# Performance work log

Measured on AMD Instinct MI355X. Metric: run time of the kernel, lower is better.

Reference implementation:

```python
import jax, jax.numpy as jnp
import numpy as np

N = 30000      # particles
E = 300000     # directed edges
H = 128        # hidden size
L = 10         # GNN layers
EMB = 16       # particle-type embedding size
T = 5          # velocity history window
NTYPES = 9
RADIUS = 0.05
OUT = 2
NODE_IN = 2 * T + 4 + EMB  # 30


def _mlp_ln(x, W1, b1, W2, b2, W3, b3, g, be):
    # Linear-ReLU-Linear-ReLU-Linear-LayerNorm (matches node/edge encoders and GraphNet blocks)
    h = jax.nn.relu(x @ W1 + b1)
    h = jax.nn.relu(h @ W2 + b2)
    h = h @ W3 + b3
    mu = jnp.mean(h, axis=-1, keepdims=True)
    var = jnp.mean((h - mu) ** 2, axis=-1, keepdims=True)
    return (h - mu) * jax.lax.rsqrt(var + 1e-5) * g + be


def setup_inputs() -> dict:
    key = jax.random.key(0)
    ks = iter(jax.random.split(key, 48))
    nx = lambda: next(ks)
    inp = {}
    inp["vel"] = jax.random.normal(nx(), (N, T, 2), jnp.float32) * 0.01
    inp["pos"] = jax.random.uniform(nx(), (N, 2), dtype=jnp.float32)
    inp["bounds"] = jnp.array([[0.0, 1.0], [0.0, 1.0]], jnp.float32)  # [dim, (lo,hi)]
    inp["tgt_pos"] = jax.random.uniform(nx(), (N, 2), dtype=jnp.float32)
    inp["particle_type"] = jax.random.randint(nx(), (N,), 0, NTYPES, jnp.int32)
    inp["nonk_mask"] = jax.random.randint(nx(), (N,), 0, 2, jnp.int32)
    inp["senders"] = jax.random.randint(nx(), (E,), 0, N, jnp.int32)
    inp["receivers"] = jax.random.randint(nx(), (E,), 0, N, jnp.int32)
    inp["emb"] = jax.random.normal(nx(), (NTYPES, EMB), jnp.float32) * 0.1

    def mlp_p(pre, din, lead=()):
        w = lambda i, o: jax.random.normal(nx(), lead + (i, o), jnp.float32) / np.sqrt(i)
        inp[pre + "_W1"] = w(din, H); inp[pre + "_b1"] = jnp.zeros(lead + (H,), jnp.float32)
        inp[pre + "_W2"] = w(H, H);   inp[pre + "_b2"] = jnp.zeros(lead + (H,), jnp.float32)
        inp[pre + "_W3"] = w(H, H);   inp[pre + "_b3"] = jnp.zeros(lead + (H,), jnp.float32)
        inp[pre + "_g"] = jnp.ones(lead + (H,), jnp.float32)
        inp[pre + "_be"] = jnp.zeros(lead + (H,), jnp.float32)

    mlp_p("ne", NODE_IN)          # node encoder
    mlp_p("ee", 3)                # edge encoder
    mlp_p("ge", 3 * H, (L,))      # per-layer edge-update MLPs
    mlp_p("gn", 2 * H, (L,))      # per-layer node-update MLPs
    inp["de_W1"] = jax.random.normal(nx(), (H, H), jnp.float32) / np.sqrt(H)
    inp["de_b1"] = jnp.zeros((H,), jnp.float32)
    inp["de_W2"] = jax.random.normal(nx(), (H, H), jnp.float32) / np.sqrt(H)
    inp["de_b2"] = jnp.zeros((H,), jnp.float32)
    inp["de_W3"] = jax.random.normal(nx(), (H, OUT), jnp.float32) / np.sqrt(H)
    inp["de_b3"] = jnp.zeros((OUT,), jnp.float32)
    return inp


def reference(vel, pos, bounds, tgt_pos, particle_type, nonk_mask, senders, receivers, emb,
              ne_W1, ne_b1, ne_W2, ne_b2, ne_W3, ne_b3, ne_g, ne_be,
              ee_W1, ee_b1, ee_W2, ee_b2, ee_W3, ee_b3, ee_g, ee_be,
              ge_W1, ge_b1, ge_W2, ge_b2, ge_W3, ge_b3, ge_g, ge_be,
              gn_W1, gn_b1, gn_W2, gn_b2, gn_W3, gn_b3, gn_g, gn_be,
              de_W1, de_b1, de_W2, de_b2, de_W3, de_b3):
    n = pos.shape[0]
    # --- construct node features ---
    vels = vel.reshape(n, -1)                                   # [N, T*2]
    dtw = jnp.concatenate([pos - bounds[:, 0], bounds[:, 1] - pos], axis=1)
    dtw = jnp.clip(dtw / RADIUS, -1.0, 1.0)                     # [N, 4]
    type_emb = emb[particle_type]                               # [N, EMB] gather
    node_attr = jnp.concatenate([vels, dtw, type_emb], axis=1)  # [N, 30]
    # --- construct edge features (senders/receivers precomputed; KD-tree is CPU-side) ---
    dist_vec = (pos[senders] - pos[receivers]) / RADIUS         # [E, 2]
    dist = jnp.linalg.norm(dist_vec, axis=1, keepdims=True)     # [E, 1]
    edge_attr = jnp.concatenate([dist_vec, dist], axis=1)       # [E, 3]
    # --- encode ---
    nodes = _mlp_ln(node_attr, ne_W1, ne_b1, ne_W2, ne_b2, ne_W3, ne_b3, ne_g, ne_be)
    edges = _mlp_ln(edge_attr, ee_W1, ee_b1, ee_W2, ee_b2, ee_W3, ee_b3, ee_g, ee_be)
    # --- process: L message-passing layers with residuals ---
    for l in range(ge_W1.shape[0]):
        e_in = jnp.concatenate([edges, nodes[senders], nodes[receivers]], axis=1)  # [E, 3H]
        edges = edges + _mlp_ln(e_in, ge_W1[l], ge_b1[l], ge_W2[l], ge_b2[l], ge_W3[l], ge_b3[l], ge_g[l], ge_be[l])
        agg = jax.ops.segment_sum(edges, receivers, num_segments=n)               # [N, H] scatter-add
        n_in = jnp.concatenate([nodes, agg], axis=1)                              # [N, 2H]
        nodes = nodes + _mlp_ln(n_in, gn_W1[l], gn_b1[l], gn_W2[l], gn_b2[l], gn_W3[l], gn_b3[l], gn_g[l], gn_be[l])
    # --- decode ---
    h = jax.nn.relu(nodes @ de_W1 + de_b1)
    h = jax.nn.relu(h @ de_W2 + de_b2)
    pred_acc = h @ de_W3 + de_b3                                 # [N, 2]
    # --- Euler integration step (out_size == 2 branch) ---
    pred_pos = pos + vel[:, -1, :] + pred_acc
    pred_pos = jnp.where(nonk_mask[:, None].astype(bool), pred_pos, tgt_pos)
    return pred_acc[:, None, :], pred_pos[:, None, :]
```

## Files before the change

kernel.cpp:

```cpp
#include <hip/hip_runtime.h>
#include <hip/hip_bf16.h>

typedef __hip_bfloat16 bf16;
typedef unsigned short u16;
typedef unsigned int u32;
typedef __attribute__((ext_vector_type(8))) short short8;
typedef __attribute__((ext_vector_type(4))) float f32x4;

#define NPART 30000
#define NEDGE 300000
#define HD 128
#define NLAYER 10
#define NFLOAT_ARRAYS 43
#define NMAT 66

__device__ __forceinline__ bool detect_bf16(const unsigned short* braw) {
    return braw[1] == 0x3F80u;
}

__device__ __forceinline__ u16 f2b(float f) {
    u32 u = __float_as_uint(f);
    u += 0x7FFFu + ((u >> 16) & 1u);
    return (u16)(u >> 16);
}
__device__ __forceinline__ u32 pack2(float a, float b) {
    return (u32)f2b(a) | ((u32)f2b(b) << 16);
}
__device__ __forceinline__ float b2flo(u32 u) { return __uint_as_float(u << 16); }
__device__ __forceinline__ float b2fhi(u32 u) { return __uint_as_float(u & 0xFFFF0000u); }

struct ConvArgs {
    const void* src[NFLOAT_ARRAYS];
    int n[NFLOAT_ARRAYS];
    int off[NFLOAT_ARRAYS];
};

__global__ __launch_bounds__(256)
void k_convert(ConvArgs a, float* __restrict__ dst, const unsigned short* __restrict__ braw)
{
    const bool isb = detect_bf16(braw);
    const int aid = blockIdx.y;
    const int n = a.n[aid];
    float* o = dst + a.off[aid];
    const int stride = gridDim.x * 256;
    int i = blockIdx.x * 256 + threadIdx.x;
    if (isb) {
        const unsigned short* s = (const unsigned short*)a.src[aid];
        for (; i < n; i += stride) {
            const unsigned int u = ((unsigned int)s[i]) << 16;
            o[i] = __uint_as_float(u);
        }
    } else {
        const float* s = (const float*)a.src[aid];
        for (; i < n; i += stride) o[i] = s[i];
    }
}

__global__ __launch_bounds__(256)
void k_hist(const int* __restrict__ rcv, int* __restrict__ counts)
{
    const int e = blockIdx.x * 256 + threadIdx.x;
    if (e < NEDGE) atomicAdd(&counts[rcv[e]], 1);
}

__global__ __launch_bounds__(1024)
void k_scan(const int* __restrict__ counts, int* __restrict__ row_ptr, int* __restrict__ cursor)
{
    __shared__ int part[1024];
    const int t = threadIdx.x;
    const int base = t * 32;
    int local[32];
    int s = 0;
#pragma unroll
    for (int k = 0; k < 32; k++) {
        const int idx = base + k;
        const int v = (idx < NPART) ? counts[idx] : 0;
        local[k] = s;
        s += v;
    }
    part[t] = s;
    __syncthreads();
    for (int off = 1; off < 1024; off <<= 1) {
        const int v = (t >= off) ? part[t - off] : 0;
        __syncthreads();
        part[t] += v;
        __syncthreads();
    }
    const int excl = (t == 0) ? 0 : part[t - 1];
#pragma unroll
    for (int k = 0; k < 32; k++) {
        const int idx = base + k;
        if (idx < NPART) {
            const int rp = excl + local[k];
            row_ptr[idx] = rp;
            cursor[idx] = rp;
        }
    }
    if (t == 0) row_ptr[NPART] = NEDGE;
}

__global__ __launch_bounds__(256)
void k_scatter(const int* __restrict__ snd, const int* __restrict__ rcv,
               int* __restrict__ cursor, int* __restrict__ snd_s, int* __restrict__ rcv_s)
{
    const int e = blockIdx.x * 256 + threadIdx.x;
    if (e < NEDGE) {
        const int r = rcv[e];
        const int p = atomicAdd(&cursor[r], 1);
        snd_s[p] = snd[e];
        rcv_s[p] = r;
    }
}

struct PackArgs {
    int src_off[NMAT];
    int dst_off[NMAT];
    int K[NMAT];
    int nks[NMAT];
};

__global__ __launch_bounds__(256)
void k_pack(const float* __restrict__ cw, u16* __restrict__ wpk, PackArgs pa)
{
    const int mid = blockIdx.y;
    const int nks = pa.nks[mid];
    const int total = nks * 4096;
    const int d = blockIdx.x * 256 + threadIdx.x;
    if (d >= total) return;
    const int j = d & 7, l = (d >> 3) & 63, t = d >> 9;
    const int ks = t % nks, mt = t / nks;
    const int hid = mt * 16 + (l & 15);
    const int k = ks * 32 + (l >> 4) * 8 + j;
    const float v = (k < pa.K[mid]) ? cw[pa.src_off[mid] + k * HD + hid] : 0.0f;
    wpk[pa.dst_off[mid] + d] = f2b(v);
}

template<int NKS, int XROW>
__device__ __forceinline__ void gemm16(const u16* __restrict__ Wp,
                                       const float* __restrict__ Bias,
                                       const u16* __restrict__ x,
                                       f32x4 acc[4][2],
                                       const int wm, const int wn,
                                       const int l15, const int lg, const int lane)
{
#pragma unroll
    for (int mt = 0; mt < 4; mt++) {
        const f32x4 bv = *(const f32x4*)(Bias + wm * 64 + mt * 16 + lg * 4);
        acc[mt][0] = bv;
        acc[mt][1] = bv;
    }
    const u16* xr0 = x + (wn * 32 + l15) * XROW + lg * 8;
    const u16* xr1 = xr0 + 16 * XROW;
    const u16* wp = Wp + (wm * 4 * NKS) * 512 + lane * 8;
#pragma unroll
    for (int ks = 0; ks < NKS; ks++) {
        const short8 b0 = *(const short8*)(xr0 + ks * 32);
        const short8 b1 = *(const short8*)(xr1 + ks * 32);
#pragma unroll
        for (int mt = 0; mt < 4; mt++) {
            const short8 a = *(const short8*)(wp + (mt * NKS + ks) * 512);
            acc[mt][0] = __builtin_amdgcn_mfma_f32_16x16x32_bf16(a, b0, acc[mt][0], 0, 0, 0);
            acc[mt][1] = __builtin_amdgcn_mfma_f32_16x16x32_bf16(a, b1, acc[mt][1], 0, 0, 0);
        }
    }
}

__device__ __forceinline__ void store_h(u16* __restrict__ h, const f32x4 acc[4][2],
                                        const int wm, const int wn, const int l15, const int lg)
{
#pragma unroll
    for (int nt = 0; nt < 2; nt++) {
        const int e = wn * 32 + nt * 16 + l15;
#pragma unroll
        for (int mt = 0; mt < 4; mt++) {
            const int hid = wm * 64 + mt * 16 + lg * 4;
            const f32x4 v = acc[mt][nt];
            const u32 lo = pack2(fmaxf(v[0], 0.0f), fmaxf(v[1], 0.0f));
            const u32 hi = pack2(fmaxf(v[2], 0.0f), fmaxf(v[3], 0.0f));
            *(uint2*)(h + e * 136 + hid) = make_uint2(lo, hi);
        }
    }
}

template<int NKS1, int XROW>
__device__ __forceinline__ void mlp_mfma(const u16* __restrict__ xs,
    u16* __restrict__ h1, u16* __restrict__ h2,
    float (*red)[2][2][16][2],
    const u16* __restrict__ W1p, const float* __restrict__ B1,
    const u16* __restrict__ W2p, const float* __restrict__ B2,
    const u16* __restrict__ W3p, const float* __restrict__ B3,
    const float* __restrict__ g, const float* __restrict__ be,
    float outv[4][2][4],
    const int wm, const int wn, const int l15, const int lg, const int lane)
{
    f32x4 acc[4][2];
    gemm16<NKS1, XROW>(W1p, B1, xs, acc, wm, wn, l15, lg, lane);
    __syncthreads();
    store_h(h1, acc, wm, wn, l15, lg);
    __syncthreads();
    gemm16<4, 136>(W2p, B2, h1, acc, wm, wn, l15, lg, lane);
    store_h(h2, acc, wm, wn, l15, lg);
    __syncthreads();
    gemm16<4, 136>(W3p, B3, h2, acc, wm, wn, l15, lg, lane);
    float ps[2], pss[2];
#pragma unroll
    for (int nt = 0; nt < 2; nt++) {
        float s = 0.0f, ss = 0.0f;
#pragma unroll
        for (int mt = 0; mt < 4; mt++) {
#pragma unroll
            for (int r = 0; r < 4; r++) {
                const float v = acc[mt][nt][r];
                s += v; ss += v * v;
            }
        }
        s += __shfl_xor(s, 16); ss += __shfl_xor(ss, 16);
        s += __shfl_xor(s, 32); ss += __shfl_xor(ss, 32);
        ps[nt] = s; pss[nt] = ss;
    }
    if (lane < 16) {
#pragma unroll
        for (int nt = 0; nt < 2; nt++) {
            red[wm][wn][nt][l15][0] = ps[nt];
            red[wm][wn][nt][l15][1] = pss[nt];
        }
    }
    __syncthreads();
#pragma unroll
    for (int nt = 0; nt < 2; nt++) {
        const float S  = red[0][wn][nt][l15][0] + red[1][wn][nt][l15][0];
        const float SS = red[0][wn][nt][l15][1] + red[1][wn][nt][l15][1];
        const float mu  = S * (1.0f / 128.0f);
        const float var = SS * (1.0f / 128.0f) - mu * mu;
        const float inv = rsqrtf(var + 1e-5f);
#pragma unroll
        for (int mt = 0; mt < 4; mt++) {
            const int hid = wm * 64 + mt * 16 + lg * 4;
            const f32x4 gv  = *(const f32x4*)(g + hid);
            const f32x4 bev = *(const f32x4*)(be + hid);
#pragma unroll
            for (int r = 0; r < 4; r++)
                outv[mt][nt][r] = (acc[mt][nt][r] - mu) * inv * gv[r] + bev[r];
        }
    }
}

__device__ __forceinline__ float nfeat(int i, int k,
    const float* __restrict__ vel, const float* __restrict__ pos,
    const float* __restrict__ bounds, const int* __restrict__ ptype,
    const float* __restrict__ emb)
{
    if (k < 10) return vel[i * 10 + k];
    if (k < 14) {
        const int q = k - 10;
        float sub;
        if (q < 2) sub = pos[i * 2 + q] - bounds[q * 2 + 0];
        else       sub = bounds[(q - 2) * 2 + 1] - pos[i * 2 + (q - 2)];
        const float dv = sub * 20.0f;
        return fminf(fmaxf(dv, -1.0f), 1.0f);
    }
    if (k < 30) return emb[ptype[i] * 16 + (k - 14)];
    return 0.0f;
}

__global__ __launch_bounds__(256)
void k_node_enc_m(const float* __restrict__ vel, const float* __restrict__ pos,
                  const float* __restrict__ bounds, const int* __restrict__ ptype,
                  const float* __restrict__ emb,
                  const u16* __restrict__ W1p, const float* __restrict__ B1,
                  const u16* __restrict__ W2p, const float* __restrict__ B2,
                  const u16* __restrict__ W3p, const float* __restrict__ B3,
                  const float* __restrict__ g, const float* __restrict__ be,
                  float* __restrict__ nodes, u16* __restrict__ nodes_bf)
{
    __shared__ __align__(16) u16 lds[17408];
    __shared__ float red[2][2][2][16][2];
    const int tid = threadIdx.x;
    const int i0 = blockIdx.x * 64;
    for (int idx = tid; idx < 1024; idx += 256) {
        const int m = idx >> 4, kk = idx & 15;
        const int i = i0 + m;
        float f0 = 0.0f, f1 = 0.0f;
        if (i < NPART) {
            f0 = nfeat(i, kk * 2 + 0, vel, pos, bounds, ptype, emb);
            f1 = nfeat(i, kk * 2 + 1, vel, pos, bounds, ptype, emb);
        }
        *(u32*)(lds + m * 40 + kk * 2) = pack2(f0, f1);
    }
    __syncthreads();
    const int lane = tid & 63, wv = tid >> 6;
    const int wm = wv >> 1, wn = wv & 1, l15 = lane & 15, lg = lane >> 4;
    float outv[4][2][4];
    mlp_mfma<1, 40>(lds, lds, lds + 8704, red, W1p, B1, W2p, B2, W3p, B3, g, be,
                    outv, wm, wn, l15, lg, lane);
#pragma unroll
    for (int nt = 0; nt < 2; nt++) {
        const int i = i0 + wn * 32 + nt * 16 + l15;
        if (i < NPART) {
#pragma unroll
            for (int mt = 0; mt < 4; mt++) {
                const int hid = wm * 64 + mt * 16 + lg * 4;
                const float4 v = make_float4(outv[mt][nt][0], outv[mt][nt][1],
                                             outv[mt][nt][2], outv[mt][nt][3]);
                *(float4*)(nodes + (size_t)i * HD + hid) = v;
                *(uint2*)(nodes_bf + (size_t)i * HD + hid) =
                    make_uint2(pack2(v.x, v.y), pack2(v.z, v.w));
            }
        }
    }
}

__global__ __launch_bounds__(256)
void k_edge_enc_m(const float* __restrict__ pos, const int* __restrict__ snd_s,
                  const int* __restrict__ rcv_s,
                  const u16* __restrict__ W1p, const float* __restrict__ B1,
                  const u16* __restrict__ W2p, const float* __restrict__ B2,
                  const u16* __restrict__ W3p, const float* __restrict__ B3,
                  const float* __restrict__ g, const float* __restrict__ be,
                  u16* __restrict__ edges_bf)
{
    __shared__ __align__(16) u16 lds[17408];
    __shared__ float red[2][2][2][16][2];
    const int tid = threadIdx.x;
    const int e0 = blockIdx.x * 64;
    for (int idx = tid; idx < 1024; idx += 256) {
        const int m = idx >> 4, kk = idx & 15;
        const int e = min(e0 + m, NEDGE - 1);
        u32 w = 0;
        if (kk < 2) {
            const int s = snd_s[e], r = rcv_s[e];
            const float dx = (pos[s * 2 + 0] - pos[r * 2 + 0]) * 20.0f;
            const float dy = (pos[s * 2 + 1] - pos[r * 2 + 1]) * 20.0f;
            if (kk == 0) w = pack2(dx, dy);
            else         w = pack2(sqrtf(dx * dx + dy * dy), 0.0f);
        }
        *(u32*)(lds + m * 40 + kk * 2) = w;
    }
    __syncthreads();
    const int lane = tid & 63, wv = tid >> 6;
    const int wm = wv >> 1, wn = wv & 1, l15 = lane & 15, lg = lane >> 4;
    float outv[4][2][4];
    mlp_mfma<1, 40>(lds, lds, lds + 8704, red, W1p, B1, W2p, B2, W3p, B3, g, be,
                    outv, wm, wn, l15, lg, lane);
#pragma unroll
    for (int nt = 0; nt < 2; nt++) {
        const int e = e0 + wn * 32 + nt * 16 + l15;
        if (e < NEDGE) {
#pragma unroll
            for (int mt = 0; mt < 4; mt++) {
                const int hid = wm * 64 + mt * 16 + lg * 4;
                *(uint2*)(edges_bf + (size_t)e * HD + hid) =
                    make_uint2(pack2(outv[mt][nt][0], outv[mt][nt][1]),
                               pack2(outv[mt][nt][2], outv[mt][nt][3]));
            }
        }
    }
}

__device__ __forceinline__ void egemm_seg32(const u16* __restrict__ Wp,
                                            const u16* __restrict__ x,
                                            f32x4 acc[2][2], const int ks0,
                                            const int wm,
                                            const int l15, const int lg, const int lane)
{
    const u16* xr0 = x + l15 * 136 + lg * 8;
    const u16* xr1 = xr0 + 16 * 136;
#pragma unroll
    for (int ks = 0; ks < 4; ks++) {
        const short8 b0 = *(const short8*)(xr0 + ks * 32);
        const short8 b1 = *(const short8*)(xr1 + ks * 32);
#pragma unroll
        for (int mt = 0; mt < 2; mt++) {
            const short8 a = *(const short8*)(Wp + (((wm * 2 + mt) * 12 + ks0 + ks) * 64 + lane) * 8);
            acc[mt][0] = __builtin_amdgcn_mfma_f32_16x16x32_bf16(a, b0, acc[mt][0], 0, 0, 0);
            acc[mt][1] = __builtin_amdgcn_mfma_f32_16x16x32_bf16(a, b1, acc[mt][1], 0, 0, 0);
        }
    }
}

__device__ __forceinline__ void egemm_h32(const u16* __restrict__ Wp,
                                          const float* __restrict__ Bias,
                                          const u16* __restrict__ x,
                                          f32x4 acc[2][2],
                                          const int wm,
                                          const int l15, const int lg, const int lane)
{
#pragma unroll
    for (int mt = 0; mt < 2; mt++) {
        const f32x4 bv = *(const f32x4*)(Bias + wm * 32 + mt * 16 + lg * 4);
        acc[mt][0] = bv;
        acc[mt][1] = bv;
    }
    const u16* xr0 = x + l15 * 136 + lg * 8;
    const u16* xr1 = xr0 + 16 * 136;
#pragma unroll
    for (int ks = 0; ks < 4; ks++) {
        const short8 b0 = *(const short8*)(xr0 + ks * 32);
        const short8 b1 = *(const short8*)(xr1 + ks * 32);
#pragma unroll
        for (int mt = 0; mt < 2; mt++) {
            const short8 a = *(const short8*)(Wp + (((wm * 2 + mt) * 4 + ks) * 64 + lane) * 8);
            acc[mt][0] = __builtin_amdgcn_mfma_f32_16x16x32_bf16(a, b0, acc[mt][0], 0, 0, 0);
            acc[mt][1] = __builtin_amdgcn_mfma_f32_16x16x32_bf16(a, b1, acc[mt][1], 0, 0, 0);
        }
    }
}

__device__ __forceinline__ void estore_h32(u16* __restrict__ h, const f32x4 acc[2][2],
                                           const int wm, const int l15, const int lg)
{
#pragma unroll
    for (int nt = 0; nt < 2; nt++) {
        const int row = nt * 16 + l15;
#pragma unroll
        for (int mt = 0; mt < 2; mt++) {
            const int hid = wm * 32 + mt * 16 + lg * 4;
            const f32x4 v = acc[mt][nt];
            const u32 lo = pack2(fmaxf(v[0], 0.0f), fmaxf(v[1], 0.0f));
            const u32 hi = pack2(fmaxf(v[2], 0.0f), fmaxf(v[3], 0.0f));
            *(uint2*)(h + row * 136 + hid) = make_uint2(lo, hi);
        }
    }
}

__global__ __launch_bounds__(256, 8)
void k_edge_layer_m(const u16* __restrict__ nodes_bf, u16* __restrict__ edges_bf,
                    float* __restrict__ agg,
                    const int* __restrict__ snd_s, const int* __restrict__ rcv_s,
                    const u16* __restrict__ W1p, const float* __restrict__ B1,
                    const u16* __restrict__ W2p, const float* __restrict__ B2,
                    const u16* __restrict__ W3p, const float* __restrict__ B3,
                    const float* __restrict__ g, const float* __restrict__ be)
{
    __shared__ __align__(16) u16 sb[2 * 4352];
    __shared__ float red[4][2][16][2];
    __shared__ int rblk[34];
    u16* b0 = sb;
    u16* b1 = sb + 4352;
    float* fout = (float*)sb;

    const int tid = threadIdx.x;
    const int e0 = blockIdx.x * 32;
    const int lane = tid & 63, wm = tid >> 6;
    const int l15 = lane & 15, lg = lane >> 4;

    if (tid < 32)       rblk[tid] = rcv_s[e0 + tid];
    else if (tid == 32) rblk[32] = (e0 > 0) ? rcv_s[e0 - 1] : -2;
    else if (tid == 33) rblk[33] = (e0 + 32 < NEDGE) ? rcv_s[e0 + 32] : -2;

    uint4 e_old[2];
#pragma unroll
    for (int t = 0; t < 2; t++) {
        const int idx = tid + t * 256;
        const int m = idx >> 4, q = idx & 15;
        e_old[t] = *(const uint4*)(edges_bf + (size_t)(e0 + m) * HD + q * 8);
        *(uint4*)(b0 + m * 136 + q * 8) = e_old[t];
    }
    uint4 st[2];
#pragma unroll
    for (int t = 0; t < 2; t++) {
        const int idx = tid + t * 256;
        const int m = idx >> 4, q = idx & 15;
        st[t] = *(const uint4*)(nodes_bf + (size_t)snd_s[e0 + m] * HD + q * 8);
    }
    __syncthreads();

    f32x4 acc[2][2];
#pragma unroll
    for (int mt = 0; mt < 2; mt++) {
        const f32x4 bv = *(const f32x4*)(B1 + wm * 32 + mt * 16 + lg * 4);
        acc[mt][0] = bv;
        acc[mt][1] = bv;
    }
    __builtin_amdgcn_s_setprio(1);
    egemm_seg32(W1p, b0, acc, 0, wm, l15, lg, lane);
    __builtin_amdgcn_s_setprio(0);
#pragma unroll
    for (int t = 0; t < 2; t++) {
        const int idx = tid + t * 256;
        const int m = idx >> 4, q = idx & 15;
        *(uint4*)(b1 + m * 136 + q * 8) = st[t];
    }
#pragma unroll
    for (int t = 0; t < 2; t++) {
        const int idx = tid + t * 256;
        const int m = idx >> 4, q = idx & 15;
        st[t] = *(const uint4*)(nodes_bf + (size_t)rcv_s[e0 + m] * HD + q * 8);
    }
    __syncthreads();

    __builtin_amdgcn_s_setprio(1);
    egemm_seg32(W1p, b1, acc, 4, wm, l15, lg, lane);
    __builtin_amdgcn_s_setprio(0);
#pragma unroll
    for (int t = 0; t < 2; t++) {
        const int idx = tid + t * 256;
        const int m = idx >> 4, q = idx & 15;
        *(uint4*)(b0 + m * 136 + q * 8) = st[t];
    }
    __syncthreads();

    __builtin_amdgcn_s_setprio(1);
    egemm_seg32(W1p, b0, acc, 8, wm, l15, lg, lane);
    __builtin_amdgcn_s_setprio(0);
    estore_h32(b1, acc, wm, l15, lg);
    __syncthreads();

    __builtin_amdgcn_s_setprio(1);
    egemm_h32(W2p, B2, b1, acc, wm, l15, lg, lane);
    __builtin_amdgcn_s_setprio(0);
    estore_h32(b0, acc, wm, l15, lg);
    __syncthreads();

    __builtin_amdgcn_s_setprio(1);
    egemm_h32(W3p, B3, b0, acc, wm, l15, lg, lane);
    __builtin_amdgcn_s_setprio(0);

    float ps[2], pss[2];
#pragma unroll
    for (int nt = 0; nt < 2; nt++) {
        float s = 0.0f, ss = 0.0f;
#pragma unroll
        for (int mt = 0; mt < 2; mt++) {
#pragma unroll
            for (int r = 0; r < 4; r++) {
                const float v = acc[mt][nt][r];
                s += v; ss += v * v;
            }
        }
        s += __shfl_xor(s, 16); ss += __shfl_xor(ss, 16);
        s += __shfl_xor(s, 32); ss += __shfl_xor(ss, 32);
        ps[nt] = s; pss[nt] = ss;
    }
    if (lane < 16) {
#pragma unroll
        for (int nt = 0; nt < 2; nt++) {
            red[wm][nt][l15][0] = ps[nt];
            red[wm][nt][l15][1] = pss[nt];
        }
    }
    __syncthreads();

#pragma unroll
    for (int nt = 0; nt < 2; nt++) {
        const float S  = red[0][nt][l15][0] + red[1][nt][l15][0]
                       + red[2][nt][l15][0] + red[3][nt][l15][0];
        const float SS = red[0][nt][l15][1] + red[1][nt][l15][1]
                       + red[2][nt][l15][1] + red[3][nt][l15][1];
        const float mu  = S * (1.0f / 128.0f);
        const float var = SS * (1.0f / 128.0f) - mu * mu;
        const float inv = rsqrtf(var + 1e-5f);
        const int row = nt * 16 + l15;
#pragma unroll
        for (int mt = 0; mt < 2; mt++) {
            const int hid = wm * 32 + mt * 16 + lg * 4;
            const f32x4 gv  = *(const f32x4*)(g + hid);
            const f32x4 bev = *(const f32x4*)(be + hid);
            f32x4 o;
#pragma unroll
            for (int r = 0; r < 4; r++)
                o[r] = (acc[mt][nt][r] - mu) * inv * gv[r] + bev[r];
            *(f32x4*)(fout + row * 132 + hid) = o;
        }
    }
    __syncthreads();

#pragma unroll
    for (int t = 0; t < 2; t++) {
        const int idx = tid + t * 256;
        const int m = idx >> 4, q = idx & 15;
        float4 lo = *(const float4*)(fout + m * 132 + q * 8);
        float4 hi = *(const float4*)(fout + m * 132 + q * 8 + 4);
        const uint4 o = e_old[t];
        lo.x += b2flo(o.x); lo.y += b2fhi(o.x);
        lo.z += b2flo(o.y); lo.w += b2fhi(o.y);
        hi.x += b2flo(o.z); hi.y += b2fhi(o.z);
        hi.z += b2flo(o.w); hi.w += b2fhi(o.w);
        *(float4*)(fout + m * 132 + q * 8) = lo;
        *(float4*)(fout + m * 132 + q * 8 + 4) = hi;
        *(uint4*)(edges_bf + (size_t)(e0 + m) * HD + q * 8) =
            make_uint4(pack2(lo.x, lo.y), pack2(lo.z, lo.w),
                       pack2(hi.x, hi.y), pack2(hi.z, hi.w));
    }
    __syncthreads();

    const int c = tid & 31;
    for (int ms = (tid >> 5); ms < 32; ms += 8) {
        const int rs = rblk[ms];
        if (ms > 0 && rblk[ms - 1] == rs) continue;
        int me = ms + 1;
        while (me < 32 && rblk[me] == rs) me++;
        float4 s = make_float4(0.0f, 0.0f, 0.0f, 0.0f);
        for (int m = ms; m < me; m++) {
            const float4 v = *(const float4*)(fout + m * 132 + c * 4);
            s.x += v.x; s.y += v.y; s.z += v.z; s.w += v.w;
        }
        float* ap = agg + (size_t)rs * HD + c * 4;
        const bool bnd = (ms == 0 && rblk[32] == rs) || (me == 32 && rblk[33] == rs);
        if (bnd) {
            atomicAdd(ap + 0, s.x); atomicAdd(ap + 1, s.y);
            atomicAdd(ap + 2, s.z); atomicAdd(ap + 3, s.w);
        } else {
            *(float4*)ap = s;
        }
    }
}

__global__ __launch_bounds__(256)
void k_node_layer_m(float* __restrict__ nodes, u16* __restrict__ nodes_bf,
                    float* __restrict__ agg,
                    const u16* __restrict__ W1p, const float* __restrict__ B1,
                    const u16* __restrict__ W2p, const float* __restrict__ B2,
                    const u16* __restrict__ W3p, const float* __restrict__ B3,
                    const float* __restrict__ g, const float* __restrict__ be)
{
    __shared__ __align__(16) u16 lds[17408];
    __shared__ float red[2][2][2][16][2];
    const int tid = threadIdx.x;
    const int i0 = blockIdx.x * 64;
    for (int idx = tid; idx < 1024; idx += 256) {
        const int m = idx >> 4, q = idx & 15;
        const int i = min(i0 + m, NPART - 1);
        const float* src = nodes + (size_t)i * HD + q * 8;
        const float4 a = *(const float4*)(src);
        const float4 b = *(const float4*)(src + 4);
        *(uint4*)(lds + m * 264 + q * 8) =
            make_uint4(pack2(a.x, a.y), pack2(a.z, a.w), pack2(b.x, b.y), pack2(b.z, b.w));
    }
    const float4 z4 = make_float4(0.0f, 0.0f, 0.0f, 0.0f);
    for (int idx = tid; idx < 1024; idx += 256) {
        const int m = idx >> 4, q = idx & 15;
        const int i = min(i0 + m, NPART - 1);
        float* src = agg + (size_t)i * HD + q * 8;
        const float4 a = *(const float4*)(src);
        const float4 b = *(const float4*)(src + 4);
        *(uint4*)(lds + m * 264 + 128 + q * 8) =
            make_uint4(pack2(a.x, a.y), pack2(a.z, a.w), pack2(b.x, b.y), pack2(b.z, b.w));
        *(float4*)(src) = z4;
        *(float4*)(src + 4) = z4;
    }
    __syncthreads();
    const int lane = tid & 63, wv = tid >> 6;
    const int wm = wv >> 1, wn = wv & 1, l15 = lane & 15, lg = lane >> 4;
    float outv[4][2][4];
    mlp_mfma<8, 264>(lds, lds, lds + 8704, red, W1p, B1, W2p, B2, W3p, B3, g, be,
                     outv, wm, wn, l15, lg, lane);
#pragma unroll
    for (int nt = 0; nt < 2; nt++) {
        const int i = i0 + wn * 32 + nt * 16 + l15;
        if (i < NPART) {
            float* np = nodes + (size_t)i * HD;
#pragma unroll
            for (int mt = 0; mt < 4; mt++) {
                const int hid = wm * 64 + mt * 16 + lg * 4;
                const float4 old = *(const float4*)(np + hid);
                const float4 nv = make_float4(old.x + outv[mt][nt][0],
                                              old.y + outv[mt][nt][1],
                                              old.z + outv[mt][nt][2],
                                              old.w + outv[mt][nt][3]);
                *(float4*)(np + hid) = nv;
                *(uint2*)(nodes_bf + (size_t)i * HD + hid) =
                    make_uint2(pack2(nv.x, nv.y), pack2(nv.z, nv.w));
            }
        }
    }
}

template<int K, int S>
__device__ __forceinline__ void gemv(const float* __restrict__ in,
                                     const float* __restrict__ W,
                                     const float* __restrict__ B,
                                     float acc[8])
{
    const int j = threadIdx.x;
    const float bb = B[j];
#pragma unroll
    for (int m = 0; m < 8; m++) acc[m] = bb;
    constexpr int K4 = (K / 4) * 4;
    for (int k = 0; k < K4; k += 4) {
        const float w0 = W[(k + 0) * HD + j];
        const float w1 = W[(k + 1) * HD + j];
        const float w2 = W[(k + 2) * HD + j];
        const float w3 = W[(k + 3) * HD + j];
#pragma unroll
        for (int m = 0; m < 8; m++) {
            const float4 x = *(const float4*)(in + m * S + k);
            float a = acc[m];
            a = fmaf(x.x, w0, a);
            a = fmaf(x.y, w1, a);
            a = fmaf(x.z, w2, a);
            a = fmaf(x.w, w3, a);
            acc[m] = a;
        }
    }
#pragma unroll
    for (int k = K4; k < K; k++) {
        const float w = W[k * HD + j];
#pragma unroll
        for (int m = 0; m < 8; m++) acc[m] = fmaf(in[m * S + k], w, acc[m]);
    }
}

__global__ __launch_bounds__(128)
void k_decoder(const float* __restrict__ nodes,
               const float* W1, const float* B1, const float* W2, const float* B2,
               const float* W3, const float* B3,
               const float* __restrict__ vel, const float* __restrict__ pos,
               const float* __restrict__ tgt, const int* __restrict__ nonk,
               const unsigned short* __restrict__ braw, void* __restrict__ d_out)
{
    __shared__ __align__(16) float xs[8 * HD];
    __shared__ __align__(16) float h1[8 * HD];
    __shared__ __align__(16) float h2[8 * HD];
    const int j = threadIdx.x;
    const int i0 = blockIdx.x * 8;
    float acc[8];
#pragma unroll
    for (int m = 0; m < 8; m++) xs[m * HD + j] = nodes[(i0 + m) * HD + j];
    __syncthreads();
    gemv<HD, HD>(xs, W1, B1, acc);
#pragma unroll
    for (int m = 0; m < 8; m++) h1[m * HD + j] = fmaxf(acc[m], 0.0f);
    __syncthreads();
    gemv<HD, HD>(h1, W2, B2, acc);
#pragma unroll
    for (int m = 0; m < 8; m++) h2[m * HD + j] = fmaxf(acc[m], 0.0f);
    __syncthreads();
    if (j < 16) {
        const int m = j >> 1, d = j & 1, i = i0 + m;
        float a = B3[d];
        for (int k = 0; k < HD; k++) a = fmaf(h2[m * HD + k], W3[k * 2 + d], a);
        float pp = pos[i * 2 + d] + vel[i * 10 + 8 + d] + a;
        if (nonk[i] == 0) pp = tgt[i * 2 + d];
        if (detect_bf16(braw)) {
            bf16* o = (bf16*)d_out;
            o[i * 2 + d] = __float2bfloat16(a);
            o[2 * NPART + i * 2 + d] = __float2bfloat16(pp);
        } else {
            float* o = (float*)d_out;
            o[i * 2 + d] = a;
            o[2 * NPART + i * 2 + d] = pp;
        }
    }
}

extern "C" void kernel_launch(void* const* d_in, const int* in_sizes, int n_in,
                              void* d_out, int out_size, void* d_ws, size_t ws_size,
                              hipStream_t stream)
{
    const int* ptype = (const int*)d_in[4];
    const int* nonk  = (const int*)d_in[5];
    const int* snd   = (const int*)d_in[6];
    const int* rcv   = (const int*)d_in[7];
    const unsigned short* braw = (const unsigned short*)d_in[2];

    int fmap[NFLOAT_ARRAYS];
    {
        int c = 0;
        fmap[c++] = 0; fmap[c++] = 1; fmap[c++] = 2; fmap[c++] = 3; fmap[c++] = 8;
        for (int i = 9; i <= 46; i++) fmap[c++] = i;
    }
    ConvArgs ca;
    const float* fp[47];
    float* cw = (float*)d_ws;
    int off = 0;
    for (int i = 0; i < NFLOAT_ARRAYS; i++) {
        ca.src[i] = d_in[fmap[i]];
        ca.n[i]   = in_sizes[fmap[i]];
        ca.off[i] = off;
        fp[fmap[i]] = cw + off;
        off += in_sizes[fmap[i]];
    }
    float* nodes = cw + ((off + 3) & ~3);
    float* agg   = nodes + (size_t)NPART * HD;
    u16* edges_bf = (u16*)(agg + (size_t)NPART * HD);
    u16* nodes_bf = edges_bf + (size_t)NEDGE * HD;
    u16* wpk = nodes_bf + (size_t)NPART * HD;

    PackArgs pa;
    int dst = 0, c = 0;
    int pk[NMAT];
    auto addm = [&](long srcoff, int K) {
        const int nk = (K + 31) / 32;
        pa.src_off[c] = (int)srcoff;
        pa.K[c] = K;
        pa.nks[c] = nk;
        pa.dst_off[c] = dst;
        pk[c] = dst;
        dst += nk * 4096;
        c++;
    };
    addm(fp[9]  - cw, 30);  addm(fp[11] - cw, 128); addm(fp[13] - cw, 128);
    addm(fp[17] - cw, 3);   addm(fp[19] - cw, 128); addm(fp[21] - cw, 128);
    for (int l = 0; l < NLAYER; l++) {
        addm(fp[25] - cw + (long)l * 384 * HD, 384);
        addm(fp[27] - cw + (long)l * HD * HD, 128);
        addm(fp[29] - cw + (long)l * HD * HD, 128);
    }
    for (int l = 0; l < NLAYER; l++) {
        addm(fp[33] - cw + (long)l * 256 * HD, 256);
        addm(fp[35] - cw + (long)l * HD * HD, 128);
        addm(fp[37] - cw + (long)l * HD * HD, 128);
    }

    int* ip = (int*)(wpk + ((dst + 7) & ~7));
    int* row_ptr = ip;            ip += NPART + 8;
    int* cursor  = ip;            ip += NPART;
    int* counts  = ip;            ip += NPART;
    int* snd_s   = ip;            ip += NEDGE;
    int* rcv_s   = ip;

    const int EBL = (NEDGE + 255) / 256;

    k_convert<<<dim3(64, NFLOAT_ARRAYS), 256, 0, stream>>>(ca, cw, braw);
    hipMemsetAsync(counts, 0, (size_t)NPART * sizeof(int), stream);
    hipMemsetAsync(agg, 0, (size_t)NPART * HD * sizeof(float), stream);
    k_hist<<<EBL, 256, 0, stream>>>(rcv, counts);
    k_scan<<<1, 1024, 0, stream>>>(counts, row_ptr, cursor);
    k_scatter<<<EBL, 256, 0, stream>>>(snd, rcv, cursor, snd_s, rcv_s);
    k_pack<<<dim3(192, NMAT), 256, 0, stream>>>(cw, wpk, pa);

    const int NB = (NPART + 63) / 64;
    const int EB = (NEDGE + 63) / 64;
    const int EB32 = NEDGE / 32;

    k_node_enc_m<<<NB, 256, 0, stream>>>(fp[0], fp[1], fp[2], ptype, fp[8],
        wpk + pk[0], fp[10], wpk + pk[1], fp[12], wpk + pk[2], fp[14],
        fp[15], fp[16], nodes, nodes_bf);
    k_edge_enc_m<<<EB, 256, 0, stream>>>(fp[1], snd_s, rcv_s,
        wpk + pk[3], fp[18], wpk + pk[4], fp[20], wpk + pk[5], fp[22],
        fp[23], fp[24], edges_bf);

    for (int l = 0; l < NLAYER; l++) {
        k_edge_layer_m<<<EB32, 256, 0, stream>>>(nodes_bf, edges_bf, agg, snd_s, rcv_s,
            wpk + pk[6 + 3 * l],  fp[26] + (size_t)l * HD,
            wpk + pk[7 + 3 * l],  fp[28] + (size_t)l * HD,
            wpk + pk[8 + 3 * l],  fp[30] + (size_t)l * HD,
            fp[31] + (size_t)l * HD, fp[32] + (size_t)l * HD);
        k_node_layer_m<<<NB, 256, 0, stream>>>(nodes, nodes_bf, agg,
            wpk + pk[36 + 3 * l], fp[34] + (size_t)l * HD,
            wpk + pk[37 + 3 * l], fp[36] + (size_t)l * HD,
            wpk + pk[38 + 3 * l], fp[38] + (size_t)l * HD,
            fp[39] + (size_t)l * HD, fp[40] + (size_t)l * HD);
    }

    k_decoder<<<NPART / 8, 128, 0, stream>>>(nodes,
        fp[41], fp[42], fp[43], fp[44], fp[45], fp[46],
        fp[0], fp[1], fp[3], nonk, braw, d_out);
}
```

Baseline: 2.219 ms.

## Replace boundary atomics with per-block partial buffers reduced in node kernel

The edge-layer kernel writes receiver segments that cross its 32-edge block boundary into a per-block boundary buffer instead of using atomicAdd into agg. The node kernel uses row_ptr to decide whether a node's sum lives in agg or must be assembled from the boundary partials of consecutive blocks. Because every agg slot is now either overwritten or ignored, the per-layer zeroing of agg and the initial memset go away. This removes float atomics and the zeroing stores, at the cost of an extra row_ptr lookup and branchy reduction in the node kernel.

```diff
diff --git a/kernel.cpp b/kernel.cpp
--- a/kernel.cpp
+++ b/kernel.cpp
@@ -425,7 +425,7 @@
 
 __global__ __launch_bounds__(256, 8)
 void k_edge_layer_m(const u16* __restrict__ nodes_bf, u16* __restrict__ edges_bf,
-                    float* __restrict__ agg,
+                    float* __restrict__ agg, float* __restrict__ bnd,
                     const int* __restrict__ snd_s, const int* __restrict__ rcv_s,
                     const u16* __restrict__ W1p, const float* __restrict__ B1,
                     const u16* __restrict__ W2p, const float* __restrict__ B2,
@@ -595,20 +595,19 @@
             const float4 v = *(const float4*)(fout + m * 132 + c * 4);
             s.x += v.x; s.y += v.y; s.z += v.z; s.w += v.w;
         }
-        float* ap = agg + (size_t)rs * HD + c * 4;
-        const bool bnd = (ms == 0 && rblk[32] == rs) || (me == 32 && rblk[33] == rs);
-        if (bnd) {
-            atomicAdd(ap + 0, s.x); atomicAdd(ap + 1, s.y);
-            atomicAdd(ap + 2, s.z); atomicAdd(ap + 3, s.w);
-        } else {
-            *(float4*)ap = s;
-        }
+        const bool extb = (ms == 0 && rblk[32] == rs);
+        const bool extf = (me == 32 && rblk[33] == rs);
+        float* ap;
+        if (!extb && !extf) ap = agg + (size_t)rs * HD + c * 4;
+        else ap = bnd + ((size_t)blockIdx.x * 2 + (extb ? 0 : 1)) * HD + c * 4;
+        *(float4*)ap = s;
     }
 }
 
 __global__ __launch_bounds__(256)
 void k_node_layer_m(float* __restrict__ nodes, u16* __restrict__ nodes_bf,
-                    float* __restrict__ agg,
+                    const float* __restrict__ agg, const float* __restrict__ bnd,
+                    const int* __restrict__ row_ptr,
                     const u16* __restrict__ W1p, const float* __restrict__ B1,
                     const u16* __restrict__ W2p, const float* __restrict__ B2,
                     const u16* __restrict__ W3p, const float* __restrict__ B3,
@@ -616,8 +615,11 @@
 {
     __shared__ __align__(16) u16 lds[17408];
     __shared__ float red[2][2][2][16][2];
+    __shared__ int rp[65];
     const int tid = threadIdx.x;
     const int i0 = blockIdx.x * 64;
+    if (tid < 65) rp[tid] = row_ptr[min(i0 + tid, NPART)];
+    __syncthreads();
     for (int idx = tid; idx < 1024; idx += 256) {
         const int m = idx >> 4, q = idx & 15;
         const int i = min(i0 + m, NPART - 1);
@@ -627,17 +629,35 @@
         *(uint4*)(lds + m * 264 + q * 8) =
             make_uint4(pack2(a.x, a.y), pack2(a.z, a.w), pack2(b.x, b.y), pack2(b.z, b.w));
     }
-    const float4 z4 = make_float4(0.0f, 0.0f, 0.0f, 0.0f);
     for (int idx = tid; idx < 1024; idx += 256) {
         const int m = idx >> 4, q = idx & 15;
-        const int i = min(i0 + m, NPART - 1);
-        float* src = agg + (size_t)i * HD + q * 8;
-        const float4 a = *(const float4*)(src);
-        const float4 b = *(const float4*)(src + 4);
+        const int i = i0 + m;
+        float4 a = make_float4(0.0f, 0.0f, 0.0f, 0.0f);
+        float4 b = make_float4(0.0f, 0.0f, 0.0f, 0.0f);
+        if (i < NPART) {
+            const int p0 = rp[m], p1 = rp[m + 1];
+            if (p1 > p0) {
+                const int b0 = p0 >> 5, b1 = (p1 - 1) >> 5;
+                if (b0 == b1) {
+                    const float* src = agg + (size_t)i * HD + q * 8;
+                    a = *(const float4*)(src);
+                    b = *(const float4*)(src + 4);
+                } else {
+                    const float* s1 = bnd + ((size_t)b0 * 2 + 1) * HD + q * 8;
+                    a = *(const float4*)(s1);
+                    b = *(const float4*)(s1 + 4);
+                    for (int bb = b0 + 1; bb <= b1; bb++) {
+                        const float* s0 = bnd + ((size_t)bb * 2 + 0) * HD + q * 8;
+                        const float4 xa = *(const float4*)(s0);
+                        const float4 xb = *(const float4*)(s0 + 4);
+                        a.x += xa.x; a.y += xa.y; a.z += xa.z; a.w += xa.w;
+                        b.x += xb.x; b.y += xb.y; b.z += xb.z; b.w += xb.w;
+                    }
+                }
+            }
+        }
         *(uint4*)(lds + m * 264 + 128 + q * 8) =
             make_uint4(pack2(a.x, a.y), pack2(a.z, a.w), pack2(b.x, b.y), pack2(b.z, b.w));
-        *(float4*)(src) = z4;
-        *(float4*)(src + 4) = z4;
     }
     __syncthreads();
     const int lane = tid & 63, wv = tid >> 6;
@@ -771,9 +791,11 @@
         fp[fmap[i]] = cw + off;
         off += in_sizes[fmap[i]];
     }
+    const int EB32 = NEDGE / 32;
     float* nodes = cw + ((off + 3) & ~3);
     float* agg   = nodes + (size_t)NPART * HD;
-    u16* edges_bf = (u16*)(agg + (size_t)NPART * HD);
+    float* bnd   = agg + (size_t)NPART * HD;
+    u16* edges_bf = (u16*)(bnd + (size_t)EB32 * 2 * HD);
     u16* nodes_bf = edges_bf + (size_t)NEDGE * HD;
     u16* wpk = nodes_bf + (size_t)NPART * HD;
 
@@ -814,7 +836,6 @@
 
     k_convert<<<dim3(64, NFLOAT_ARRAYS), 256, 0, stream>>>(ca, cw, braw);
     hipMemsetAsync(counts, 0, (size_t)NPART * sizeof(int), stream);
-    hipMemsetAsync(agg, 0, (size_t)NPART * HD * sizeof(float), stream);
     k_hist<<<EBL, 256, 0, stream>>>(rcv, counts);
     k_scan<<<1, 1024, 0, stream>>>(counts, row_ptr, cursor);
     k_scatter<<<EBL, 256, 0, stream>>>(snd, rcv, cursor, snd_s, rcv_s);
@@ -822,7 +843,6 @@
 
     const int NB = (NPART + 63) / 64;
     const int EB = (NEDGE + 63) / 64;
-    const int EB32 = NEDGE / 32;
 
     k_node_enc_m<<<NB, 256, 0, stream>>>(fp[0], fp[1], fp[2], ptype, fp[8],
         wpk + pk[0], fp[10], wpk + pk[1], fp[12], wpk + pk[2], fp[14],
@@ -832,12 +852,12 @@
         fp[23], fp[24], edges_bf);
 
     for (int l = 0; l < NLAYER; l++) {
-        k_edge_layer_m<<<EB32, 256, 0, stream>>>(nodes_bf, edges_bf, agg, snd_s, rcv_s,
+        k_edge_layer_m<<<EB32, 256, 0, stream>>>(nodes_bf, edges_bf, agg, bnd, snd_s, rcv_s,
             wpk + pk[6 + 3 * l],  fp[26] + (size_t)l * HD,
             wpk + pk[7 + 3 * l],  fp[28] + (size_t)l * HD,
             wpk + pk[8 + 3 * l],  fp[30] + (size_t)l * HD,
             fp[31] + (size_t)l * HD, fp[32] + (size_t)l * HD);
-        k_node_layer_m<<<NB, 256, 0, stream>>>(nodes, nodes_bf, agg,
+        k_node_layer_m<<<NB, 256, 0, stream>>>(nodes, nodes_bf, agg, bnd, row_ptr,
             wpk + pk[36 + 3 * l], fp[34] + (size_t)l * HD,
             wpk + pk[37 + 3 * l], fp[36] + (size_t)l * HD,
             wpk + pk[38 + 3 * l], fp[38] + (size_t)l * HD,
```

Measured after the change: 2.207 ms. No clear change (-0.6%).
